# Kernel optimization log

Measured on AMD Instinct MI355X. Metric: run time of the kernel, lower is better.

## Reference

```python
import jax, jax.numpy as jnp
import numpy as np

DIM = 180
HEADS = 6
HEAD_DIM = DIM // HEADS
SCALE = HEAD_DIM ** (-0.5)
BW, N, K = 8192, 64, 16


def setup_inputs() -> dict:
    key = jax.random.key(0)
    ks = jax.random.split(key, 6)
    return {
        "x": jax.random.normal(ks[0], (BW, N, DIM), dtype=jnp.float32),
        "bpe_windows": jax.random.normal(ks[1], (BW, N, K), dtype=jnp.float32),
        "qkv_w": jax.random.normal(ks[2], (3 * DIM, DIM), dtype=jnp.float32) * 0.05,
        "qkv_b": jax.random.normal(ks[3], (3 * DIM,), dtype=jnp.float32) * 0.05,
        "proj_w": jax.random.normal(ks[4], (DIM, DIM), dtype=jnp.float32) * 0.05,
        "proj_b": jax.random.normal(ks[5], (DIM,), dtype=jnp.float32) * 0.05,
        "tau": jnp.ones((HEADS, 1, 1), dtype=jnp.float32),
    }


def reference(x, bpe_windows, qkv_w, qkv_b, proj_w, proj_b, tau):
    B_, n, C = x.shape
    # qkv projection -> (3, B_, H, N, hd)
    qkv = (x @ qkv_w.T + qkv_b).reshape(B_, n, 3, HEADS, HEAD_DIM)
    qkv = jnp.transpose(qkv, (2, 0, 3, 1, 4))
    q, k, v = qkv[0], qkv[1], qkv[2]
    q = q * SCALE
    attn = jnp.einsum("bhid,bhjd->bhij", q, k)  # (B_, H, N, N)
    # geodesic bias from BPE embeddings: d_B(i,j) = ||bpe_i - bpe_j||_2
    diff = bpe_windows[:, :, None, :] - bpe_windows[:, None, :, :]  # (B_, N, N, K)
    d_B = jnp.sqrt(jnp.sum(diff * diff, axis=-1))  # (B_, N, N)
    log_W_geo = -d_B[:, None, :, :] / jnp.clip(tau, 1e-6)[None]  # (B_, H, N, N)
    attn = jax.nn.softmax(attn + log_W_geo, axis=-1)
    out = jnp.einsum("bhij,bhjd->bhid", attn, v)  # (B_, H, N, hd)
    out = jnp.transpose(out, (0, 2, 1, 3)).reshape(B_, n, C)
    return out @ proj_w.T + proj_b
```

## Files before the change

kernel.cpp:

```cpp
#include <hip/hip_runtime.h>
#include <hip/hip_fp16.h>
#include <math.h>

typedef __attribute__((ext_vector_type(8))) short short8b;
typedef __attribute__((ext_vector_type(4))) float f32x4;
typedef __attribute__((ext_vector_type(4))) unsigned short ushort4b;
typedef __attribute__((ext_vector_type(2))) unsigned short ushort2b;

#define NWIN 8192
#define NT   512
#define SCALE 0.18257418583505536f

#define XB_P 200
#define QK_P 200
#define VT_P 72
#define DB_P 68
#define ATT_P 184

#define OFF_XB  0
#define OFF_QK  25600
#define OFF_VT  51200
#define OFF_DB  65024
#define OFF_BPE 73728
#define LDS_BYTES 78848

#define WK 192

__device__ __forceinline__ unsigned short f2bf(float f) {
    union { float f; unsigned int u; } v; v.f = f;
    return (unsigned short)((v.u + 0x7FFFu + ((v.u >> 16) & 1u)) >> 16);
}

__global__ void prep_weights(const float* __restrict__ qkv_w,
                             const float* __restrict__ proj_w,
                             unsigned short* __restrict__ wqr,
                             unsigned short* __restrict__ wpr)
{
    const int idx = blockIdx.x * 256 + threadIdx.x;
    if (idx < 540 * WK) {
        const int r = idx / WK, k = idx % WK;
        const int seg = r / 30, dd = r % 30;
        const int which = seg / 6, hh = seg % 6;
        float v = 0.f;
        if (k < 180)
            v = qkv_w[(which * 180 + hh * 30 + dd) * 180 + k];
        wqr[idx] = f2bf(v);
    }
    const int j = idx - 540 * WK;
    if (j >= 0 && j < WK * WK) {
        const int r = j / WK, k = j % WK;
        float v = 0.f;
        if (r < 180 && k < 180)
            v = proj_w[r * 180 + k];
        wpr[j] = f2bf(v);
    }
}

__global__ void __launch_bounds__(NT, 4)
waga_mfma(const float* __restrict__ x,
          const float* __restrict__ bpe,
          const unsigned short* __restrict__ wqr,
          const unsigned short* __restrict__ wpr,
          const float* __restrict__ qkv_b,
          const float* __restrict__ proj_b,
          const float* __restrict__ tau,
          float* __restrict__ out)
{
    extern __shared__ char smem[];
    unsigned short* xb   = (unsigned short*)(smem + OFF_XB);
    unsigned short* qk   = (unsigned short*)(smem + OFF_QK);
    unsigned short* vT   = (unsigned short*)(smem + OFF_VT);
    unsigned short* dBs  = (unsigned short*)(smem + OFF_DB);
    float*          bpes = (float*)(smem + OFF_BPE);

    const int b = blockIdx.x;
    const int t = threadIdx.x;
    const int w = t >> 6;
    const int l = t & 63;
    const int lr = l & 15;
    const int g  = l >> 4;

    unsigned short* attg = (unsigned short*)((char*)out + (size_t)b * 46080 + 22528);

    if (t < 192) {
        const int n = t / 3, c = t % 3;
        *reinterpret_cast<uint2*>(xb + n * XB_P + 180 + 4 * c) = make_uint2(0u, 0u);
    } else if (t < 256) {
        const int n = t - 192;
        ushort4b z = {0, 0, 0, 0};
        *reinterpret_cast<ushort4b*>(attg + n * ATT_P + 180) = z;
    }
    {
        const float* xw = x + (size_t)b * 11520;
        for (int i = t; i < 64 * 45; i += NT) {
            const int n = i / 45, c4 = i % 45;
            const float4 v = *reinterpret_cast<const float4*>(xw + i * 4);
            ushort4b o;
            o[0] = f2bf(v.x); o[1] = f2bf(v.y); o[2] = f2bf(v.z); o[3] = f2bf(v.w);
            *reinterpret_cast<ushort4b*>(xb + n * XB_P + c4 * 4) = o;
        }
    }
    if (t < 256) {
        const float4 v = *reinterpret_cast<const float4*>(bpe + (size_t)b * 1024 + t * 4);
        *reinterpret_cast<float4*>(bpes + (t >> 2) * 20 + (t & 3) * 4) = v;
    }
    __syncthreads();

    {
        const int ti = t >> 4, tj = t & 15;
        float acc0[4] = {0.f, 0.f, 0.f, 0.f};
        float acc1[4] = {0.f, 0.f, 0.f, 0.f};
        #pragma unroll
        for (int k4 = 0; k4 < 4; ++k4) {
            const float4 a0 = *reinterpret_cast<const float4*>(bpes + ti * 20 + 4 * k4);
            const float4 a1 = *reinterpret_cast<const float4*>(bpes + (ti + 32) * 20 + 4 * k4);
            #pragma unroll
            for (int e = 0; e < 4; ++e) {
                const float4 bb = *reinterpret_cast<const float4*>(bpes + (tj + 16 * e) * 20 + 4 * k4);
                float d;
                d = a0.x - bb.x; acc0[e] += d * d;
                d = a0.y - bb.y; acc0[e] += d * d;
                d = a0.z - bb.z; acc0[e] += d * d;
                d = a0.w - bb.w; acc0[e] += d * d;
                d = a1.x - bb.x; acc1[e] += d * d;
                d = a1.y - bb.y; acc1[e] += d * d;
                d = a1.z - bb.z; acc1[e] += d * d;
                d = a1.w - bb.w; acc1[e] += d * d;
            }
        }
        #pragma unroll
        for (int e = 0; e < 4; ++e) {
            dBs[ti * DB_P + tj + 16 * e] =
                __half_as_ushort(__float2half_rn(sqrtf(acc0[e])));
            dBs[(ti + 32) * DB_P + tj + 16 * e] =
                __half_as_ushort(__float2half_rn(sqrtf(acc1[e])));
        }
    }

    for (int pass = 0; pass < 2; ++pass) {
        if (pass) __syncthreads();

        {
            f32x4 acc[3][4];
            const unsigned short* wrow[3];
            bool has[3], arow_ok[3];
            int whichv[3], hhl[3], halfv[3];
            #pragma unroll
            for (int ti = 0; ti < 3; ++ti) {
                const int tl = w + 8 * ti;
                has[ti] = (tl < 18);
                const int tls = has[ti] ? tl : 0;
                const int segl = tls >> 1;
                halfv[ti] = tls & 1;
                whichv[ti] = segl / 3;
                hhl[ti] = segl % 3;
                const int hg = 3 * pass + hhl[ti];
                const int wseg = whichv[ti] * 6 + hg;
                const int ddr = halfv[ti] * 16 + lr;
                arow_ok[ti] = (ddr < 30);
                wrow[ti] = wqr + (size_t)(wseg * 30 + (arow_ok[ti] ? ddr : 0)) * WK;
                const int ddb = halfv[ti] * 16 + g * 4;
                const int cbase = whichv[ti] * 180 + hg * 30;
                f32x4 binit;
                #pragma unroll
                for (int i = 0; i < 4; ++i)
                    binit[i] = (ddb + i < 30) ? qkv_b[cbase + ddb + i] : 0.f;
                #pragma unroll
                for (int mt = 0; mt < 4; ++mt) acc[ti][mt] = binit;
            }
            #pragma unroll
            for (int kk = 0; kk < 6; ++kk) {
                short8b xf[4];
                #pragma unroll
                for (int mt = 0; mt < 4; ++mt)
                    xf[mt] = *reinterpret_cast<const short8b*>(
                        xb + (mt * 16 + lr) * XB_P + kk * 32 + g * 8);
                #pragma unroll
                for (int ti = 0; ti < 3; ++ti) {
                    if (!has[ti]) continue;
                    short8b wfv;
                    if (arow_ok[ti])
                        wfv = *reinterpret_cast<const short8b*>(wrow[ti] + kk * 32 + g * 8);
                    else
                        wfv = short8b{0, 0, 0, 0, 0, 0, 0, 0};
                    #pragma unroll
                    for (int mt = 0; mt < 4; ++mt)
                        acc[ti][mt] = __builtin_amdgcn_mfma_f32_16x16x32_bf16(
                            wfv, xf[mt], acc[ti][mt], 0, 0, 0);
                }
            }
            #pragma unroll
            for (int ti = 0; ti < 3; ++ti) {
                if (!has[ti]) continue;
                const int ddb = halfv[ti] * 16 + g * 4;
                #pragma unroll
                for (int mt = 0; mt < 4; ++mt) {
                    const int tok = mt * 16 + lr;
                    float v0 = acc[ti][mt][0], v1 = acc[ti][mt][1];
                    float v2 = acc[ti][mt][2], v3 = acc[ti][mt][3];
                    if (whichv[ti] == 0) { v0 *= SCALE; v1 *= SCALE; v2 *= SCALE; v3 *= SCALE; }
                    if (whichv[ti] < 2) {
                        ushort4b o;
                        o[0] = f2bf(v0); o[1] = f2bf(v1); o[2] = f2bf(v2); o[3] = f2bf(v3);
                        *reinterpret_cast<ushort4b*>(
                            qk + tok * QK_P + hhl[ti] * 64 + whichv[ti] * 32 + ddb) = o;
                    } else {
                        const int c = (tok & 32) + ((tok >> 2) & 3) * 8 + ((tok >> 4) & 1) * 4 + (tok & 3);
                        unsigned short* vb = vT + hhl[ti] * 2304 + ddb * VT_P + c;
                        vb[0 * VT_P] = f2bf(v0);
                        vb[1 * VT_P] = f2bf(v1);
                        vb[2 * VT_P] = f2bf(v2);
                        vb[3 * VT_P] = f2bf(v3);
                    }
                }
            }
        }
        __syncthreads();

        for (int u = w; u < 12; u += 8) {
            const int hh = u >> 2, mt = u & 3;
            const int h = 3 * pass + hh;
            const unsigned short* qkh = qk + hh * 64;
            const short8b qf = *reinterpret_cast<const short8b*>(
                qkh + (mt * 16 + lr) * QK_P + g * 8);
            short8b kf[4];
            #pragma unroll
            for (int jt = 0; jt < 4; ++jt)
                kf[jt] = *reinterpret_cast<const short8b*>(
                    qkh + (jt * 16 + lr) * QK_P + 32 + g * 8);
            short8b vf[2][2];
            #pragma unroll
            for (int ntd = 0; ntd < 2; ++ntd)
                #pragma unroll
                for (int ks = 0; ks < 2; ++ks)
                    vf[ntd][ks] = *reinterpret_cast<const short8b*>(
                        vT + hh * 2304 + (ntd * 16 + lr) * VT_P + ks * 32 + g * 8);
            const float itau = 1.f / fmaxf(tau[h], 1e-6f);
            f32x4 s[4];
            #pragma unroll
            for (int jt = 0; jt < 4; ++jt) {
                const ushort4b du = *reinterpret_cast<const ushort4b*>(
                    dBs + (mt * 16 + lr) * DB_P + jt * 16 + g * 4);
                #pragma unroll
                for (int i = 0; i < 4; ++i)
                    s[jt][i] = -itau * __half2float(__ushort_as_half(du[i]));
            }
            #pragma unroll
            for (int jt = 0; jt < 4; ++jt)
                s[jt] = __builtin_amdgcn_mfma_f32_16x16x32_bf16(kf[jt], qf, s[jt], 0, 0, 0);
            float mx = s[0][0];
            #pragma unroll
            for (int jt = 0; jt < 4; ++jt)
                #pragma unroll
                for (int i = 0; i < 4; ++i) mx = fmaxf(mx, s[jt][i]);
            mx = fmaxf(mx, __shfl_xor(mx, 16));
            mx = fmaxf(mx, __shfl_xor(mx, 32));
            float sum = 0.f;
            #pragma unroll
            for (int jt = 0; jt < 4; ++jt)
                #pragma unroll
                for (int i = 0; i < 4; ++i) {
                    const float p = __expf(s[jt][i] - mx);
                    s[jt][i] = p; sum += p;
                }
            sum += __shfl_xor(sum, 16);
            sum += __shfl_xor(sum, 32);
            const float inv = 1.f / sum;
            short8b pb[2];
            #pragma unroll
            for (int ks = 0; ks < 2; ++ks) {
                pb[ks][0] = (short)f2bf(s[2 * ks][0] * inv);
                pb[ks][1] = (short)f2bf(s[2 * ks][1] * inv);
                pb[ks][2] = (short)f2bf(s[2 * ks][2] * inv);
                pb[ks][3] = (short)f2bf(s[2 * ks][3] * inv);
                pb[ks][4] = (short)f2bf(s[2 * ks + 1][0] * inv);
                pb[ks][5] = (short)f2bf(s[2 * ks + 1][1] * inv);
                pb[ks][6] = (short)f2bf(s[2 * ks + 1][2] * inv);
                pb[ks][7] = (short)f2bf(s[2 * ks + 1][3] * inv);
            }
            const int tok = mt * 16 + lr;
            #pragma unroll
            for (int ntd = 0; ntd < 2; ++ntd) {
                f32x4 o = {0.f, 0.f, 0.f, 0.f};
                o = __builtin_amdgcn_mfma_f32_16x16x32_bf16(vf[ntd][0], pb[0], o, 0, 0, 0);
                o = __builtin_amdgcn_mfma_f32_16x16x32_bf16(vf[ntd][1], pb[1], o, 0, 0, 0);
                const int col = h * 30 + ntd * 16 + g * 4;
                unsigned short* dst = attg + tok * ATT_P + col;
                if (ntd == 0 || g < 3) {
                    ushort4b ov;
                    ov[0] = f2bf(o[0]); ov[1] = f2bf(o[1]);
                    ov[2] = f2bf(o[2]); ov[3] = f2bf(o[3]);
                    *reinterpret_cast<ushort4b*>(dst) = ov;
                } else {
                    ushort2b ov;
                    ov[0] = f2bf(o[0]); ov[1] = f2bf(o[1]);
                    *reinterpret_cast<ushort2b*>(dst) = ov;
                }
            }
        }
    }
    __syncthreads();

    {
        const int mt = w & 3;
        const int ntb = (w >> 2) * 6;
        short8b attf[6];
        #pragma unroll
        for (int kk = 0; kk < 6; ++kk) {
            if (kk == 5 && g == 3)
                attf[kk] = short8b{0, 0, 0, 0, 0, 0, 0, 0};
            else
                attf[kk] = *reinterpret_cast<const short8b*>(
                    attg + (mt * 16 + lr) * ATT_P + kk * 32 + g * 8);
        }
        f32x4 pacc[6];
        #pragma unroll
        for (int q6 = 0; q6 < 6; ++q6) {
            const int nt = ntb + q6;
            const unsigned short* wrow = wpr + (size_t)(nt * 16 + lr) * WK;
            const int cb = nt * 16 + g * 4;
            f32x4 acc;
            #pragma unroll
            for (int i = 0; i < 4; ++i)
                acc[i] = (cb + i < 180) ? proj_b[cb + i] : 0.f;
            #pragma unroll
            for (int kk = 0; kk < 6; ++kk) {
                const short8b wf = *reinterpret_cast<const short8b*>(wrow + kk * 32 + g * 8);
                acc = __builtin_amdgcn_mfma_f32_16x16x32_bf16(wf, attf[kk], acc, 0, 0, 0);
            }
            pacc[q6] = acc;
        }
        __syncthreads();
        #pragma unroll
        for (int q6 = 0; q6 < 6; ++q6) {
            const int nt = ntb + q6;
            const int cb = nt * 16 + g * 4;
            if (cb < 177) {
                const int tok = mt * 16 + lr;
                *reinterpret_cast<float4*>(out + ((size_t)b * 64 + tok) * 180 + cb) =
                    make_float4(pacc[q6][0], pacc[q6][1], pacc[q6][2], pacc[q6][3]);
            }
        }
    }
}

extern "C" void kernel_launch(void* const* d_in, const int* in_sizes, int n_in,
                              void* d_out, int out_size, void* d_ws, size_t ws_size,
                              hipStream_t stream) {
    (void)in_sizes; (void)n_in; (void)out_size; (void)ws_size;
    const float* x      = (const float*)d_in[0];
    const float* bpe    = (const float*)d_in[1];
    const float* qkv_w  = (const float*)d_in[2];
    const float* qkv_b  = (const float*)d_in[3];
    const float* proj_w = (const float*)d_in[4];
    const float* proj_b = (const float*)d_in[5];
    const float* tau    = (const float*)d_in[6];

    unsigned short* wqr = (unsigned short*)d_ws;
    unsigned short* wpr = wqr + 540 * WK;

    prep_weights<<<(540 * WK + WK * WK + 255) / 256, 256, 0, stream>>>(
        qkv_w, proj_w, wqr, wpr);

    (void)hipFuncSetAttribute((const void*)waga_mfma,
                              hipFuncAttributeMaxDynamicSharedMemorySize,
                              LDS_BYTES);
    waga_mfma<<<NWIN, NT, LDS_BYTES, stream>>>(x, bpe, wqr, wpr, qkv_b, proj_b, tau,
                                               (float*)d_out);
}
```

Before: 728.5 us.

## Compute geodesic distances via MFMA Gram matrix and use packed bf16 conversions

Replaces the precomputed pairwise BPE distance table with a per-tile MFMA computation of the Gram matrix on bf16 BPE rows. Distances are then recovered as sqrt(|a|^2+|b|^2-2ab), with the diagonal forced to zero and negatives clamped. This removes the scalar O(N^2 K) distance pass, one barrier and the fp16 distance LDS buffer, which lowers LDS use. It also switches to hardware packed bf16 conversions and tree-shaped max/sum reductions in the softmax. The cost is some accuracy in the distances, since bf16 Gram terms suffer cancellation.

After: 834.3 us. 1.15x slower.

```diff
diff --git a/kernel.cpp b/kernel.cpp
--- a/kernel.cpp
+++ b/kernel.cpp
@@ -1,5 +1,5 @@
 #include <hip/hip_runtime.h>
-#include <hip/hip_fp16.h>
+#include <hip/hip_bf16.h>
 #include <math.h>
 
 typedef __attribute__((ext_vector_type(8))) short short8b;
@@ -14,21 +14,27 @@
 #define XB_P 200
 #define QK_P 200
 #define VT_P 72
-#define DB_P 68
+#define BPE_P 36
 #define ATT_P 184
 
 #define OFF_XB  0
 #define OFF_QK  25600
 #define OFF_VT  51200
-#define OFF_DB  65024
-#define OFF_BPE 73728
-#define LDS_BYTES 78848
+#define OFF_BPE 65024
+#define OFF_N   69632
+#define LDS_BYTES 69888
 
 #define WK 192
 
-__device__ __forceinline__ unsigned short f2bf(float f) {
-    union { float f; unsigned int u; } v; v.f = f;
-    return (unsigned short)((v.u + 0x7FFFu + ((v.u >> 16) & 1u)) >> 16);
+__device__ __forceinline__ unsigned int bf2pk(float lo, float hi) {
+    union { __hip_bfloat162 h; unsigned int u; } cv;
+    cv.h = __float22bfloat162_rn(make_float2(lo, hi));
+    return cv.u;
+}
+__device__ __forceinline__ unsigned short bf1(float v) {
+    union { __hip_bfloat16 h; unsigned short u; } cv;
+    cv.h = __float2bfloat16(v);
+    return cv.u;
 }
 
 __global__ void prep_weights(const float* __restrict__ qkv_w,
@@ -44,7 +50,7 @@
         float v = 0.f;
         if (k < 180)
             v = qkv_w[(which * 180 + hh * 30 + dd) * 180 + k];
-        wqr[idx] = f2bf(v);
+        wqr[idx] = bf1(v);
     }
     const int j = idx - 540 * WK;
     if (j >= 0 && j < WK * WK) {
@@ -52,7 +58,7 @@
         float v = 0.f;
         if (r < 180 && k < 180)
             v = proj_w[r * 180 + k];
-        wpr[j] = f2bf(v);
+        wpr[j] = bf1(v);
     }
 }
 
@@ -70,8 +76,8 @@
     unsigned short* xb   = (unsigned short*)(smem + OFF_XB);
     unsigned short* qk   = (unsigned short*)(smem + OFF_QK);
     unsigned short* vT   = (unsigned short*)(smem + OFF_VT);
-    unsigned short* dBs  = (unsigned short*)(smem + OFF_DB);
-    float*          bpes = (float*)(smem + OFF_BPE);
+    unsigned short* bpeB = (unsigned short*)(smem + OFF_BPE);
+    float*          nv   = (float*)(smem + OFF_N);
 
     const int b = blockIdx.x;
     const int t = threadIdx.x;
@@ -89,53 +95,37 @@
         const int n = t - 192;
         ushort4b z = {0, 0, 0, 0};
         *reinterpret_cast<ushort4b*>(attg + n * ATT_P + 180) = z;
+    } else if (t < 512) {
+        const int i = t - 256;
+        const int n = i >> 2, c4 = i & 3;
+        ushort4b z = {0, 0, 0, 0};
+        *reinterpret_cast<ushort4b*>(bpeB + n * BPE_P + 16 + 4 * c4) = z;
     }
     {
         const float* xw = x + (size_t)b * 11520;
         for (int i = t; i < 64 * 45; i += NT) {
             const int n = i / 45, c4 = i % 45;
             const float4 v = *reinterpret_cast<const float4*>(xw + i * 4);
-            ushort4b o;
-            o[0] = f2bf(v.x); o[1] = f2bf(v.y); o[2] = f2bf(v.z); o[3] = f2bf(v.w);
-            *reinterpret_cast<ushort4b*>(xb + n * XB_P + c4 * 4) = o;
+            *reinterpret_cast<uint2*>(xb + n * XB_P + c4 * 4) =
+                make_uint2(bf2pk(v.x, v.y), bf2pk(v.z, v.w));
         }
     }
     if (t < 256) {
         const float4 v = *reinterpret_cast<const float4*>(bpe + (size_t)b * 1024 + t * 4);
-        *reinterpret_cast<float4*>(bpes + (t >> 2) * 20 + (t & 3) * 4) = v;
-    }
-    __syncthreads();
-
-    {
-        const int ti = t >> 4, tj = t & 15;
-        float acc0[4] = {0.f, 0.f, 0.f, 0.f};
-        float acc1[4] = {0.f, 0.f, 0.f, 0.f};
+        *reinterpret_cast<uint2*>(bpeB + (t >> 2) * BPE_P + (t & 3) * 4) =
+            make_uint2(bf2pk(v.x, v.y), bf2pk(v.z, v.w));
+    }
+    if (t < 64) {
+        const float* bp = bpe + (size_t)b * 1024 + t * 16;
+        float s = 0.f;
         #pragma unroll
         for (int k4 = 0; k4 < 4; ++k4) {
-            const float4 a0 = *reinterpret_cast<const float4*>(bpes + ti * 20 + 4 * k4);
-            const float4 a1 = *reinterpret_cast<const float4*>(bpes + (ti + 32) * 20 + 4 * k4);
-            #pragma unroll
-            for (int e = 0; e < 4; ++e) {
-                const float4 bb = *reinterpret_cast<const float4*>(bpes + (tj + 16 * e) * 20 + 4 * k4);
-                float d;
-                d = a0.x - bb.x; acc0[e] += d * d;
-                d = a0.y - bb.y; acc0[e] += d * d;
-                d = a0.z - bb.z; acc0[e] += d * d;
-                d = a0.w - bb.w; acc0[e] += d * d;
-                d = a1.x - bb.x; acc1[e] += d * d;
-                d = a1.y - bb.y; acc1[e] += d * d;
-                d = a1.z - bb.z; acc1[e] += d * d;
-                d = a1.w - bb.w; acc1[e] += d * d;
-            }
-        }
-        #pragma unroll
-        for (int e = 0; e < 4; ++e) {
-            dBs[ti * DB_P + tj + 16 * e] =
-                __half_as_ushort(__float2half_rn(sqrtf(acc0[e])));
-            dBs[(ti + 32) * DB_P + tj + 16 * e] =
-                __half_as_ushort(__float2half_rn(sqrtf(acc1[e])));
-        }
-    }
+            const float4 v = *reinterpret_cast<const float4*>(bp + 4 * k4);
+            s += v.x * v.x + v.y * v.y + v.z * v.z + v.w * v.w;
+        }
+        nv[t] = s;
+    }
+    __syncthreads();
 
     for (int pass = 0; pass < 2; ++pass) {
         if (pass) __syncthreads();
@@ -200,17 +190,16 @@
                     float v2 = acc[ti][mt][2], v3 = acc[ti][mt][3];
                     if (whichv[ti] == 0) { v0 *= SCALE; v1 *= SCALE; v2 *= SCALE; v3 *= SCALE; }
                     if (whichv[ti] < 2) {
-                        ushort4b o;
-                        o[0] = f2bf(v0); o[1] = f2bf(v1); o[2] = f2bf(v2); o[3] = f2bf(v3);
-                        *reinterpret_cast<ushort4b*>(
-                            qk + tok * QK_P + hhl[ti] * 64 + whichv[ti] * 32 + ddb) = o;
+                        *reinterpret_cast<uint2*>(
+                            qk + tok * QK_P + hhl[ti] * 64 + whichv[ti] * 32 + ddb) =
+                            make_uint2(bf2pk(v0, v1), bf2pk(v2, v3));
                     } else {
                         const int c = (tok & 32) + ((tok >> 2) & 3) * 8 + ((tok >> 4) & 1) * 4 + (tok & 3);
                         unsigned short* vb = vT + hhl[ti] * 2304 + ddb * VT_P + c;
-                        vb[0 * VT_P] = f2bf(v0);
-                        vb[1 * VT_P] = f2bf(v1);
-                        vb[2 * VT_P] = f2bf(v2);
-                        vb[3 * VT_P] = f2bf(v3);
+                        vb[0 * VT_P] = bf1(v0);
+                        vb[1 * VT_P] = bf1(v1);
+                        vb[2 * VT_P] = bf1(v2);
+                        vb[3 * VT_P] = bf1(v3);
                     }
                 }
             }
@@ -220,9 +209,10 @@
         for (int u = w; u < 12; u += 8) {
             const int hh = u >> 2, mt = u & 3;
             const int h = 3 * pass + hh;
+            const int tok = mt * 16 + lr;
             const unsigned short* qkh = qk + hh * 64;
             const short8b qf = *reinterpret_cast<const short8b*>(
-                qkh + (mt * 16 + lr) * QK_P + g * 8);
+                qkh + tok * QK_P + g * 8);
             short8b kf[4];
             #pragma unroll
             for (int jt = 0; jt < 4; ++jt)
@@ -235,66 +225,72 @@
                 for (int ks = 0; ks < 2; ++ks)
                     vf[ntd][ks] = *reinterpret_cast<const short8b*>(
                         vT + hh * 2304 + (ntd * 16 + lr) * VT_P + ks * 32 + g * 8);
+            const short8b btf = *reinterpret_cast<const short8b*>(
+                bpeB + tok * BPE_P + g * 8);
+            const f32x4 zero4 = {0.f, 0.f, 0.f, 0.f};
+            f32x4 g2[4];
+            #pragma unroll
+            for (int jt = 0; jt < 4; ++jt) {
+                const short8b baf = *reinterpret_cast<const short8b*>(
+                    bpeB + (jt * 16 + lr) * BPE_P + g * 8);
+                g2[jt] = __builtin_amdgcn_mfma_f32_16x16x32_bf16(baf, btf, zero4, 0, 0, 0);
+            }
             const float itau = 1.f / fmaxf(tau[h], 1e-6f);
+            const float ntok = nv[tok];
             f32x4 s[4];
             #pragma unroll
             for (int jt = 0; jt < 4; ++jt) {
-                const ushort4b du = *reinterpret_cast<const ushort4b*>(
-                    dBs + (mt * 16 + lr) * DB_P + jt * 16 + g * 4);
-                #pragma unroll
-                for (int i = 0; i < 4; ++i)
-                    s[jt][i] = -itau * __half2float(__ushort_as_half(du[i]));
+                const f32x4 nj = *reinterpret_cast<const f32x4*>(nv + jt * 16 + g * 4);
+                #pragma unroll
+                for (int i = 0; i < 4; ++i) {
+                    const int j = jt * 16 + g * 4 + i;
+                    float d2 = fmaf(-2.f, g2[jt][i], ntok + nj[i]);
+                    d2 = (j == tok) ? 0.f : fmaxf(d2, 0.f);
+                    s[jt][i] = -itau * __builtin_sqrtf(d2);
+                }
             }
             #pragma unroll
             for (int jt = 0; jt < 4; ++jt)
                 s[jt] = __builtin_amdgcn_mfma_f32_16x16x32_bf16(kf[jt], qf, s[jt], 0, 0, 0);
-            float mx = s[0][0];
-            #pragma unroll
-            for (int jt = 0; jt < 4; ++jt)
-                #pragma unroll
-                for (int i = 0; i < 4; ++i) mx = fmaxf(mx, s[jt][i]);
+            float m4[4], a4[4];
+            #pragma unroll
+            for (int i = 0; i < 4; ++i)
+                m4[i] = fmaxf(fmaxf(s[0][i], s[1][i]), fmaxf(s[2][i], s[3][i]));
+            float mx = fmaxf(fmaxf(m4[0], m4[1]), fmaxf(m4[2], m4[3]));
             mx = fmaxf(mx, __shfl_xor(mx, 16));
             mx = fmaxf(mx, __shfl_xor(mx, 32));
-            float sum = 0.f;
             #pragma unroll
             for (int jt = 0; jt < 4; ++jt)
                 #pragma unroll
-                for (int i = 0; i < 4; ++i) {
-                    const float p = __expf(s[jt][i] - mx);
-                    s[jt][i] = p; sum += p;
-                }
+                for (int i = 0; i < 4; ++i)
+                    s[jt][i] = __expf(s[jt][i] - mx);
+            #pragma unroll
+            for (int i = 0; i < 4; ++i)
+                a4[i] = (s[0][i] + s[1][i]) + (s[2][i] + s[3][i]);
+            float sum = (a4[0] + a4[1]) + (a4[2] + a4[3]);
             sum += __shfl_xor(sum, 16);
             sum += __shfl_xor(sum, 32);
             const float inv = 1.f / sum;
-            short8b pb[2];
+            union { short8b v; unsigned int u[4]; } pb[2];
             #pragma unroll
             for (int ks = 0; ks < 2; ++ks) {
-                pb[ks][0] = (short)f2bf(s[2 * ks][0] * inv);
-                pb[ks][1] = (short)f2bf(s[2 * ks][1] * inv);
-                pb[ks][2] = (short)f2bf(s[2 * ks][2] * inv);
-                pb[ks][3] = (short)f2bf(s[2 * ks][3] * inv);
-                pb[ks][4] = (short)f2bf(s[2 * ks + 1][0] * inv);
-                pb[ks][5] = (short)f2bf(s[2 * ks + 1][1] * inv);
-                pb[ks][6] = (short)f2bf(s[2 * ks + 1][2] * inv);
-                pb[ks][7] = (short)f2bf(s[2 * ks + 1][3] * inv);
-            }
-            const int tok = mt * 16 + lr;
+                pb[ks].u[0] = bf2pk(s[2 * ks][0] * inv, s[2 * ks][1] * inv);
+                pb[ks].u[1] = bf2pk(s[2 * ks][2] * inv, s[2 * ks][3] * inv);
+                pb[ks].u[2] = bf2pk(s[2 * ks + 1][0] * inv, s[2 * ks + 1][1] * inv);
+                pb[ks].u[3] = bf2pk(s[2 * ks + 1][2] * inv, s[2 * ks + 1][3] * inv);
+            }
             #pragma unroll
             for (int ntd = 0; ntd < 2; ++ntd) {
                 f32x4 o = {0.f, 0.f, 0.f, 0.f};
-                o = __builtin_amdgcn_mfma_f32_16x16x32_bf16(vf[ntd][0], pb[0], o, 0, 0, 0);
-                o = __builtin_amdgcn_mfma_f32_16x16x32_bf16(vf[ntd][1], pb[1], o, 0, 0, 0);
+                o = __builtin_amdgcn_mfma_f32_16x16x32_bf16(vf[ntd][0], pb[0].v, o, 0, 0, 0);
+                o = __builtin_amdgcn_mfma_f32_16x16x32_bf16(vf[ntd][1], pb[1].v, o, 0, 0, 0);
                 const int col = h * 30 + ntd * 16 + g * 4;
                 unsigned short* dst = attg + tok * ATT_P + col;
                 if (ntd == 0 || g < 3) {
-                    ushort4b ov;
-                    ov[0] = f2bf(o[0]); ov[1] = f2bf(o[1]);
-                    ov[2] = f2bf(o[2]); ov[3] = f2bf(o[3]);
-                    *reinterpret_cast<ushort4b*>(dst) = ov;
+                    *reinterpret_cast<uint2*>(dst) =
+                        make_uint2(bf2pk(o[0], o[1]), bf2pk(o[2], o[3]));
                 } else {
-                    ushort2b ov;
-                    ov[0] = f2bf(o[0]); ov[1] = f2bf(o[1]);
-                    *reinterpret_cast<ushort2b*>(dst) = ov;
+                    *reinterpret_cast<unsigned int*>(dst) = bf2pk(o[0], o[1]);
                 }
             }
         }
```
